# Kernel tuning notes

Measured on AMD Instinct MI355X. Metric: run time of the kernel, lower is better.

Reference implementation:

```python
import jax, jax.numpy as jnp
import numpy as np

N_NODES = 20000
N_EDGES = 320000
D = 512
CENTERS = 8
N_CLASSES = 128


def setup_inputs() -> dict:
    key = jax.random.key(0)
    k1, k2, k3, k4 = jax.random.split(key, 4)
    h = jax.random.normal(k1, (N_NODES, D), dtype=jnp.float32)
    edge_index = jax.random.randint(k2, (2, N_EDGES), 0, N_NODES, dtype=jnp.int32)
    Ws = jax.random.normal(k3, (CENTERS, D), dtype=jnp.float32) * 0.05
    Wt = jax.random.normal(k4, (CENTERS, N_CLASSES, D), dtype=jnp.float32) * 0.05
    return {"h": h, "edge_index": edge_index, "Ws": Ws, "Wt": Wt}


def reference(h, edge_index, Ws, Wt):
    N = h.shape[0]
    # add self loops (add_self_loops)
    loops = jnp.arange(N, dtype=edge_index.dtype)
    src = jnp.concatenate([edge_index[0], loops])
    dst = jnp.concatenate([edge_index[1], loops])
    # scatter-mean aggregation: agg[i] = mean_{(j->i)} h[j]
    summed = jax.ops.segment_sum(h[src], dst, num_segments=N)  # [N, D]
    cnt = jax.ops.segment_sum(jnp.ones_like(dst, dtype=h.dtype), dst, num_segments=N)
    hm = summed / cnt[:, None]  # cnt >= 1 due to self loops
    # router: argmax over structure-token scores
    scores = hm @ Ws.T                         # [N, CENTERS]
    route = jnp.argmax(scores, axis=1)         # [N]
    # hard-routed per-expert linear (compute all experts, select routed one)
    all_out = jnp.einsum('nd,cod->nco', hm, Wt)  # [N, CENTERS, N_CLASSES]
    out = jnp.take_along_axis(all_out, route[:, None, None], axis=1)[:, 0, :]
    return out
```

## Files before the change

kernel.cpp:

```cpp
#include <hip/hip_runtime.h>

#define DIM    512
#define NCLS   128
#define NCENT  8
#define TM     64
#define WSLOT  64
#define NB     64
#define KC2    64
#define KP2    72

typedef unsigned short ushort_t;
typedef unsigned int   uint_t;
typedef __attribute__((ext_vector_type(8))) short bf16x8;
typedef __attribute__((ext_vector_type(4))) float f32x4;

static __device__ __forceinline__ ushort_t f2bf(float f) {
    uint_t x = __float_as_uint(f);
    uint_t r = (x + 0x7fffu + ((x >> 16) & 1u)) >> 16;
    return (ushort_t)r;
}
static __device__ __forceinline__ float bf_lo(uint_t w) {
    return __uint_as_float(w << 16);
}
static __device__ __forceinline__ float bf_hi(uint_t w) {
    return __uint_as_float(w & 0xffff0000u);
}


__global__ __launch_bounds__(256) void prep_kernel(const float* __restrict__ h,
                                                   const float* __restrict__ Ws,
                                                   const float* __restrict__ Wt,
                                                   ushort_t* __restrict__ hb,
                                                   float* __restrict__ q,
                                                   ushort_t* __restrict__ wtb,
                                                   int N, int nprep, int total8) {
    if ((int)blockIdx.x >= nprep) {
        int i = (blockIdx.x - nprep) * 256 + threadIdx.x;
        if (i < total8) {
            const float* src = Wt + (size_t)i * 8;
            float4 a = *(const float4*)src;
            float4 b = *(const float4*)(src + 4);
            union { ushort_t us[8]; uint4 v; } pk;
            pk.us[0] = f2bf(a.x); pk.us[1] = f2bf(a.y);
            pk.us[2] = f2bf(a.z); pk.us[3] = f2bf(a.w);
            pk.us[4] = f2bf(b.x); pk.us[5] = f2bf(b.y);
            pk.us[6] = f2bf(b.z); pk.us[7] = f2bf(b.w);
            *(uint4*)(wtb + (size_t)i * 8) = pk.v;
        }
        return;
    }
    int wid = (blockIdx.x * 256 + threadIdx.x) >> 6;
    int lane = threadIdx.x & 63;
    if (wid >= N) return;

    const float* row = h + (size_t)wid * DIM + lane * 8;
    float4 a = *(const float4*)row;
    float4 b = *(const float4*)(row + 4);
    float fa[8] = {a.x, a.y, a.z, a.w, b.x, b.y, b.z, b.w};

    union { ushort_t us[8]; uint4 v; } pk;
    #pragma unroll
    for (int i = 0; i < 8; ++i) pk.us[i] = f2bf(fa[i]);
    *(uint4*)(hb + (size_t)wid * DIM + lane * 8) = pk.v;

    float qv = 0.f;
    #pragma unroll
    for (int c = 0; c < NCENT; ++c) {
        const float* w = Ws + c * DIM + lane * 8;
        float4 w0 = *(const float4*)w;
        float4 w1 = *(const float4*)(w + 4);
        float p = fa[0]*w0.x + fa[1]*w0.y + fa[2]*w0.z + fa[3]*w0.w
                + fa[4]*w1.x + fa[5]*w1.y + fa[6]*w1.z + fa[7]*w1.w;
        #pragma unroll
        for (int s = 32; s > 0; s >>= 1) p += __shfl_xor(p, s, 64);
        if (lane == c) qv = p;
    }
    if (lane < NCENT) q[(size_t)wid * NCENT + lane] = qv;
}


__global__ __launch_bounds__(256) void scatter_pad_kernel(const int* __restrict__ src,
                                                          const int* __restrict__ dst,
                                                          int* __restrict__ cnt,
                                                          int* __restrict__ slots, int E) {
    int i = blockIdx.x * 256 + threadIdx.x;
    if (i < E) {
        int d = dst[i];
        int k = atomicAdd(&cnt[d], 1);
        if (k < WSLOT) slots[(size_t)d * WSLOT + k] = src[i];
    }
}


__global__ __launch_bounds__(256) void gather_route_kernel(
        const ushort_t* __restrict__ hb, const int* __restrict__ cnt,
        const int* __restrict__ slots, const float* __restrict__ q,
        ushort_t* __restrict__ hmb, int* __restrict__ route, int N) {
    int wid = (blockIdx.x * 256 + threadIdx.x) >> 6;
    int lane = threadIdx.x & 63;
    if (wid >= N) return;

    int cn = cnt[wid]; if (cn > WSLOT) cn = WSLOT;
    int myslot = (lane < cn) ? slots[(size_t)wid * WSLOT + lane] : 0;

    float qs[NCENT];
    if (lane < cn) {
        const float* qr = q + (size_t)myslot * NCENT;
        float4 q0 = *(const float4*)qr;
        float4 q1 = *(const float4*)(qr + 4);
        qs[0]=q0.x; qs[1]=q0.y; qs[2]=q0.z; qs[3]=q0.w;
        qs[4]=q1.x; qs[5]=q1.y; qs[6]=q1.z; qs[7]=q1.w;
    } else {
        #pragma unroll
        for (int c = 0; c < NCENT; ++c) qs[c] = 0.f;
    }

    float acc[8];
    {
        uint4 u = *(const uint4*)(hb + (size_t)wid * DIM + lane * 8);
        acc[0] = bf_lo(u.x); acc[1] = bf_hi(u.x);
        acc[2] = bf_lo(u.y); acc[3] = bf_hi(u.y);
        acc[4] = bf_lo(u.z); acc[5] = bf_hi(u.z);
        acc[6] = bf_lo(u.w); acc[7] = bf_hi(u.w);
    }
    int j = 0;
    for (; j + 8 <= cn; j += 8) {
        uint4 u[8];
        #pragma unroll
        for (int k = 0; k < 8; ++k) {
            int s = __shfl(myslot, j + k, 64);
            u[k] = *(const uint4*)(hb + (size_t)s * DIM + lane * 8);
        }
        #pragma unroll
        for (int k = 0; k < 8; ++k) {
            acc[0] += bf_lo(u[k].x); acc[1] += bf_hi(u[k].x);
            acc[2] += bf_lo(u[k].y); acc[3] += bf_hi(u[k].y);
            acc[4] += bf_lo(u[k].z); acc[5] += bf_hi(u[k].z);
            acc[6] += bf_lo(u[k].w); acc[7] += bf_hi(u[k].w);
        }
    }
    for (; j < cn; ++j) {
        int s = __shfl(myslot, j, 64);
        uint4 u = *(const uint4*)(hb + (size_t)s * DIM + lane * 8);
        acc[0] += bf_lo(u.x); acc[1] += bf_hi(u.x);
        acc[2] += bf_lo(u.y); acc[3] += bf_hi(u.y);
        acc[4] += bf_lo(u.z); acc[5] += bf_hi(u.z);
        acc[6] += bf_lo(u.w); acc[7] += bf_hi(u.w);
    }
    float inv = 1.0f / (float)(cn + 1);
    union { ushort_t us[8]; uint4 v; } pk;
    #pragma unroll
    for (int k = 0; k < 8; ++k) pk.us[k] = f2bf(acc[k] * inv);
    *(uint4*)(hmb + (size_t)wid * DIM + lane * 8) = pk.v;

    #pragma unroll
    for (int c = 0; c < NCENT; ++c) {
        float v = qs[c];
        #pragma unroll
        for (int s = 32; s > 0; s >>= 1) v += __shfl_xor(v, s, 64);
        qs[c] = v;
    }
    if (lane == 0) {
        const float* qn = q + (size_t)wid * NCENT;
        int best = 0; float bv = qs[0] + qn[0];
        #pragma unroll
        for (int c = 1; c < NCENT; ++c) {
            float v = qs[c] + qn[c];
            if (v > bv) { bv = v; best = c; }
        }
        route[wid] = best;
    }
}


__global__ __launch_bounds__(256) void route_hist_kernel(const int* __restrict__ route,
                                                         int* __restrict__ bhist, int N) {
    __shared__ int lh[NCENT];
    int t = threadIdx.x;
    if (t < NCENT) lh[t] = 0;
    __syncthreads();
    for (int i = blockIdx.x * 256 + t; i < N; i += NB * 256)
        atomicAdd(&lh[route[i]], 1);
    __syncthreads();
    if (t < NCENT) bhist[blockIdx.x * NCENT + t] = lh[t];
}


__global__ __launch_bounds__(512) void scan_bins_kernel(const int* __restrict__ bhist,
                                                        int* __restrict__ bbase,
                                                        int* __restrict__ goff,
                                                        int* __restrict__ tloff) {
    __shared__ int s[NCENT][NB];
    __shared__ int go[NCENT + 1], tl[NCENT + 1];
    int t = threadIdx.x;
    int b = t >> 3, c = t & 7;
    int v = bhist[b * NCENT + c];
    s[c][b] = v;
    __syncthreads();
    for (int st = 1; st < NB; st <<= 1) {
        int a = (b >= st) ? s[c][b - st] : 0;
        __syncthreads();
        s[c][b] += a;
        __syncthreads();
    }
    if (t == 0) {
        int g = 0, tt = 0;
        for (int cc = 0; cc < NCENT; ++cc) {
            go[cc] = g; tl[cc] = tt;
            int gc = s[cc][NB - 1];
            g += gc; tt += (gc + TM - 1) / TM;
        }
        go[NCENT] = g; tl[NCENT] = tt;
    }
    __syncthreads();
    bbase[b * NCENT + c] = go[c] + s[c][b] - v;
    if (t < NCENT + 1) { goff[t] = go[t]; tloff[t] = tl[t]; }
}


__global__ __launch_bounds__(256) void group_scatter2_kernel(
        const int* __restrict__ route, const int* __restrict__ bbase,
        int* __restrict__ nlist, int N) {
    __shared__ int lcur[NCENT];
    int t = threadIdx.x;
    if (t < NCENT) lcur[t] = bbase[blockIdx.x * NCENT + t];
    __syncthreads();
    for (int i = blockIdx.x * 256 + t; i < N; i += NB * 256) {
        int p = atomicAdd(&lcur[route[i]], 1);
        nlist[p] = i;
    }
}


__global__ __launch_bounds__(256) void gemm_mfma_kernel(
        const ushort_t* __restrict__ hmb, const int* __restrict__ nlist,
        const int* __restrict__ goff, const int* __restrict__ tloff,
        const ushort_t* __restrict__ wtb, float* __restrict__ out) {
    __shared__ ushort_t a_s[TM * KP2];
    __shared__ ushort_t b_s[NCLS * KP2];
    __shared__ int nl_s[TM];

    int b = blockIdx.x;
    if (b >= tloff[NCENT]) return;
    int c = 0;
    while (b >= tloff[c + 1]) ++c;
    int row0 = goff[c] + (b - tloff[c]) * TM;
    int mrows = goff[c + 1] - row0; if (mrows > TM) mrows = TM;

    int tid = threadIdx.x;
    int wv = tid >> 6;
    int lane = tid & 63;

    if (tid < TM) nl_s[tid] = nlist[row0 + (tid < mrows ? tid : mrows - 1)];
    __syncthreads();

    f32x4 acc[8];
    #pragma unroll
    for (int t = 0; t < 8; ++t) acc[t] = (f32x4){0.f, 0.f, 0.f, 0.f};

    const ushort_t* wt_c = wtb + (size_t)c * NCLS * DIM;

    for (int k0 = 0; k0 < DIM; k0 += KC2) {
        #pragma unroll
        for (int r = 0; r < 2; ++r) {
            int idx = tid + 256 * r;
            int row = idx >> 3;
            int kq = (idx & 7) * 8;
            int nd = nl_s[row];
            uint4 v = *(const uint4*)(hmb + (size_t)nd * DIM + k0 + kq);
            *(uint4*)&a_s[row * KP2 + kq] = v;
        }
        #pragma unroll
        for (int r = 0; r < 4; ++r) {
            int idx = tid + 256 * r;
            int row = idx >> 3;
            int kq = (idx & 7) * 8;
            uint4 v = *(const uint4*)(wt_c + (size_t)row * DIM + k0 + kq);
            *(uint4*)&b_s[row * KP2 + kq] = v;
        }
        __syncthreads();
        #pragma unroll
        for (int s = 0; s < 2; ++s) {
            int kof = s * 32 + (lane >> 4) * 8;
            bf16x8 af = *(const bf16x8*)&a_s[(wv * 16 + (lane & 15)) * KP2 + kof];
            #pragma unroll
            for (int t = 0; t < 8; ++t) {
                bf16x8 bf = *(const bf16x8*)&b_s[(t * 16 + (lane & 15)) * KP2 + kof];
                acc[t] = __builtin_amdgcn_mfma_f32_16x16x32_bf16(af, bf, acc[t], 0, 0, 0);
            }
        }
        __syncthreads();
    }

    #pragma unroll
    for (int r4 = 0; r4 < 4; ++r4) {
        int row = wv * 16 + (lane >> 4) * 4 + r4;
        if (row < mrows) {
            int nd = nl_s[row];
            float* orow = out + (size_t)nd * NCLS + (lane & 15);
            #pragma unroll
            for (int t = 0; t < 8; ++t)
                orow[t * 16] = acc[t][r4];
        }
    }
}


__global__ __launch_bounds__(256) void node_kernel(const float* __restrict__ h,
                                                   const int* __restrict__ cnt,
                                                   const int* __restrict__ slots,
                                                   const float* __restrict__ Ws,
                                                   const float* __restrict__ Wt,
                                                   float* __restrict__ out) {
    int node = blockIdx.x;
    int t = threadIdx.x;
    __shared__ float hm[DIM];
    __shared__ float sc[NCENT];
    __shared__ int route_s;

    int d0 = t * 2;
    float2 acc = *(const float2*)(h + (size_t)node * DIM + d0);
    int cn = cnt[node]; if (cn > WSLOT) cn = WSLOT;
    const int* sl = slots + (size_t)node * WSLOT;
    for (int j = 0; j < cn; ++j) {
        float2 v = *(const float2*)(h + (size_t)sl[j] * DIM + d0);
        acc.x += v.x; acc.y += v.y;
    }
    float inv = 1.0f / (float)(cn + 1);
    hm[d0] = acc.x * inv; hm[d0 + 1] = acc.y * inv;
    __syncthreads();
    if (t < NCENT) {
        const float* w = Ws + t * DIM;
        float s = 0.f;
        for (int d = 0; d < DIM; d += 4) {
            float4 a = *(const float4*)(&hm[d]);
            float4 b = *(const float4*)(w + d);
            s += a.x * b.x + a.y * b.y + a.z * b.z + a.w * b.w;
        }
        sc[t] = s;
    }
    __syncthreads();
    if (t == 0) {
        int best = 0; float bv = sc[0];
        #pragma unroll
        for (int c = 1; c < NCENT; ++c)
            if (sc[c] > bv) { bv = sc[c]; best = c; }
        route_s = best;
    }
    __syncthreads();
    int route = route_s;
    if (t < NCLS) {
        const float* w = Wt + ((size_t)route * NCLS + t) * DIM;
        float s = 0.f;
        for (int d = 0; d < DIM; d += 4) {
            float4 a = *(const float4*)(&hm[d]);
            float4 b = *(const float4*)(w + d);
            s += a.x * b.x + a.y * b.y + a.z * b.z + a.w * b.w;
        }
        out[(size_t)node * NCLS + t] = s;
    }
}


extern "C" void kernel_launch(void* const* d_in, const int* in_sizes, int n_in,
                              void* d_out, int out_size, void* d_ws, size_t ws_size,
                              hipStream_t stream) {
    const float* h   = (const float*)d_in[0];
    const int*   ei  = (const int*)d_in[1];
    const float* Ws  = (const float*)d_in[2];
    const float* Wt  = (const float*)d_in[3];
    float*       out = (float*)d_out;

    int N = in_sizes[0] / DIM;
    int E = in_sizes[1] / 2;
    int wt_elems = in_sizes[3];
    const int* esrc = ei;
    const int* edst = ei + E;

    int* wsp    = (int*)d_ws;
    int* cnt    = wsp;
    int* route  = cnt + N;
    int* goff   = route + N;
    int* tloff  = goff + NCENT + 1;
    int* bhist  = tloff + NCENT + 1;
    int* bbase  = bhist + NB * NCENT;
    int* nlist  = bbase + NB * NCENT;
    int* slots  = nlist + N;
    size_t iw   = (size_t)(3 * N) + 2 * (NCENT + 1) + 2 * NB * NCENT
                + (size_t)N * WSLOT;
    size_t q_off  = ((iw * 4 + 255) & ~(size_t)255);
    float* q    = (float*)((char*)d_ws + q_off);
    size_t hb_off = ((q_off + (size_t)N * NCENT * 4 + 255) & ~(size_t)255);
    ushort_t* hb = (ushort_t*)((char*)d_ws + hb_off);
    size_t hmb_off = ((hb_off + (size_t)N * DIM * 2 + 255) & ~(size_t)255);
    ushort_t* hmb = (ushort_t*)((char*)d_ws + hmb_off);
    size_t wtb_off = ((hmb_off + (size_t)N * DIM * 2 + 255) & ~(size_t)255);
    ushort_t* wtb = (ushort_t*)((char*)d_ws + wtb_off);
    size_t need = wtb_off + (size_t)wt_elems * 2;

    hipMemsetAsync(cnt, 0, (size_t)N * sizeof(int), stream);

    if (ws_size >= need) {
        int nprep = (N + 3) / 4;
        int total8 = wt_elems / 8;
        int nwt = (total8 + 255) / 256;
        prep_kernel<<<nprep + nwt, 256, 0, stream>>>(h, Ws, Wt, hb, q, wtb,
                                                     N, nprep, total8);
        scatter_pad_kernel<<<(E + 255) / 256, 256, 0, stream>>>(esrc, edst, cnt, slots, E);
        gather_route_kernel<<<(N + 3) / 4, 256, 0, stream>>>(hb, cnt, slots, q,
                                                             hmb, route, N);
        route_hist_kernel<<<NB, 256, 0, stream>>>(route, bhist, N);
        scan_bins_kernel<<<1, 512, 0, stream>>>(bhist, bbase, goff, tloff);
        group_scatter2_kernel<<<NB, 256, 0, stream>>>(route, bbase, nlist, N);
        int maxtiles = N / TM + NCENT + 1;
        gemm_mfma_kernel<<<maxtiles, 256, 0, stream>>>(hmb, nlist, goff, tloff, wtb, out);
    } else {
        scatter_pad_kernel<<<(E + 255) / 256, 256, 0, stream>>>(esrc, edst, cnt, slots, E);
        node_kernel<<<N, 256, 0, stream>>>(h, cnt, slots, Ws, Wt, out);
    }
}
```

Baseline: 114.3 us.

## Fuse edge scatter into prep and scan into group scatter; deepen gather prefetch

Merges the edge-slot scatter into the prep kernel as extra blocks, and folds the single-block bin scan into the per-block group-scatter kernel, where each block redundantly recomputes the prefix. Together these remove two kernel launches and their serialization gaps. The gather kernel also issues up to 16 neighbor row loads up front before accumulating, to raise memory-level parallelism for typical degrees (~17). The costs are more registers in the gather kernel and redundant scan work in each of the 64 blocks.

```diff
diff --git a/kernel.cpp b/kernel.cpp
--- a/kernel.cpp
+++ b/kernel.cpp
@@ -27,36 +27,46 @@
 }
 
 
-__global__ __launch_bounds__(256) void prep_kernel(const float* __restrict__ h,
-                                                   const float* __restrict__ Ws,
-                                                   const float* __restrict__ Wt,
-                                                   ushort_t* __restrict__ hb,
-                                                   float* __restrict__ q,
-                                                   ushort_t* __restrict__ wtb,
-                                                   int N, int nprep, int total8) {
-    if ((int)blockIdx.x >= nprep) {
-        int i = (blockIdx.x - nprep) * 256 + threadIdx.x;
+__global__ __launch_bounds__(256) void fused_prep_kernel(
+        const float* __restrict__ h, const float* __restrict__ Ws,
+        const float* __restrict__ Wt, const int* __restrict__ esrc,
+        const int* __restrict__ edst, ushort_t* __restrict__ hb,
+        float* __restrict__ q, ushort_t* __restrict__ wtb,
+        int* __restrict__ cnt, int* __restrict__ slots,
+        int N, int E, int nprep, int nwt, int total8) {
+    int b = blockIdx.x;
+    if (b >= nprep + nwt) {
+        int i = (b - nprep - nwt) * 256 + threadIdx.x;
+        if (i < E) {
+            int d = edst[i];
+            int k = atomicAdd(&cnt[d], 1);
+            if (k < WSLOT) slots[(size_t)d * WSLOT + k] = esrc[i];
+        }
+        return;
+    }
+    if (b >= nprep) {
+        int i = (b - nprep) * 256 + threadIdx.x;
         if (i < total8) {
             const float* src = Wt + (size_t)i * 8;
             float4 a = *(const float4*)src;
-            float4 b = *(const float4*)(src + 4);
+            float4 bb = *(const float4*)(src + 4);
             union { ushort_t us[8]; uint4 v; } pk;
-            pk.us[0] = f2bf(a.x); pk.us[1] = f2bf(a.y);
-            pk.us[2] = f2bf(a.z); pk.us[3] = f2bf(a.w);
-            pk.us[4] = f2bf(b.x); pk.us[5] = f2bf(b.y);
-            pk.us[6] = f2bf(b.z); pk.us[7] = f2bf(b.w);
+            pk.us[0] = f2bf(a.x);  pk.us[1] = f2bf(a.y);
+            pk.us[2] = f2bf(a.z);  pk.us[3] = f2bf(a.w);
+            pk.us[4] = f2bf(bb.x); pk.us[5] = f2bf(bb.y);
+            pk.us[6] = f2bf(bb.z); pk.us[7] = f2bf(bb.w);
             *(uint4*)(wtb + (size_t)i * 8) = pk.v;
         }
         return;
     }
-    int wid = (blockIdx.x * 256 + threadIdx.x) >> 6;
+    int wid = (b * 256 + threadIdx.x) >> 6;
     int lane = threadIdx.x & 63;
     if (wid >= N) return;
 
     const float* row = h + (size_t)wid * DIM + lane * 8;
     float4 a = *(const float4*)row;
-    float4 b = *(const float4*)(row + 4);
-    float fa[8] = {a.x, a.y, a.z, a.w, b.x, b.y, b.z, b.w};
+    float4 bb = *(const float4*)(row + 4);
+    float fa[8] = {a.x, a.y, a.z, a.w, bb.x, bb.y, bb.z, bb.w};
 
     union { ushort_t us[8]; uint4 v; } pk;
     #pragma unroll
@@ -76,19 +86,6 @@
         if (lane == c) qv = p;
     }
     if (lane < NCENT) q[(size_t)wid * NCENT + lane] = qv;
-}
-
-
-__global__ __launch_bounds__(256) void scatter_pad_kernel(const int* __restrict__ src,
-                                                          const int* __restrict__ dst,
-                                                          int* __restrict__ cnt,
-                                                          int* __restrict__ slots, int E) {
-    int i = blockIdx.x * 256 + threadIdx.x;
-    if (i < E) {
-        int d = dst[i];
-        int k = atomicAdd(&cnt[d], 1);
-        if (k < WSLOT) slots[(size_t)d * WSLOT + k] = src[i];
-    }
 }
 
 
@@ -115,37 +112,52 @@
         for (int c = 0; c < NCENT; ++c) qs[c] = 0.f;
     }
 
+    uint4 su = *(const uint4*)(hb + (size_t)wid * DIM + lane * 8);
+    uint4 u[16];
+    int m = cn < 16 ? cn : 16;
+    #pragma unroll
+    for (int k = 0; k < 16; ++k) {
+        int s = __shfl(myslot, k, 64);
+        if (k < m) u[k] = *(const uint4*)(hb + (size_t)s * DIM + lane * 8);
+    }
+
     float acc[8];
-    {
-        uint4 u = *(const uint4*)(hb + (size_t)wid * DIM + lane * 8);
-        acc[0] = bf_lo(u.x); acc[1] = bf_hi(u.x);
-        acc[2] = bf_lo(u.y); acc[3] = bf_hi(u.y);
-        acc[4] = bf_lo(u.z); acc[5] = bf_hi(u.z);
-        acc[6] = bf_lo(u.w); acc[7] = bf_hi(u.w);
-    }
-    int j = 0;
-    for (; j + 8 <= cn; j += 8) {
-        uint4 u[8];
-        #pragma unroll
-        for (int k = 0; k < 8; ++k) {
-            int s = __shfl(myslot, j + k, 64);
-            u[k] = *(const uint4*)(hb + (size_t)s * DIM + lane * 8);
-        }
-        #pragma unroll
-        for (int k = 0; k < 8; ++k) {
+    acc[0] = bf_lo(su.x); acc[1] = bf_hi(su.x);
+    acc[2] = bf_lo(su.y); acc[3] = bf_hi(su.y);
+    acc[4] = bf_lo(su.z); acc[5] = bf_hi(su.z);
+    acc[6] = bf_lo(su.w); acc[7] = bf_hi(su.w);
+    #pragma unroll
+    for (int k = 0; k < 16; ++k) {
+        if (k < m) {
             acc[0] += bf_lo(u[k].x); acc[1] += bf_hi(u[k].x);
             acc[2] += bf_lo(u[k].y); acc[3] += bf_hi(u[k].y);
             acc[4] += bf_lo(u[k].z); acc[5] += bf_hi(u[k].z);
             acc[6] += bf_lo(u[k].w); acc[7] += bf_hi(u[k].w);
         }
     }
+    int j = 16;
+    for (; j + 8 <= cn; j += 8) {
+        uint4 v[8];
+        #pragma unroll
+        for (int k = 0; k < 8; ++k) {
+            int s = __shfl(myslot, j + k, 64);
+            v[k] = *(const uint4*)(hb + (size_t)s * DIM + lane * 8);
+        }
+        #pragma unroll
+        for (int k = 0; k < 8; ++k) {
+            acc[0] += bf_lo(v[k].x); acc[1] += bf_hi(v[k].x);
+            acc[2] += bf_lo(v[k].y); acc[3] += bf_hi(v[k].y);
+            acc[4] += bf_lo(v[k].z); acc[5] += bf_hi(v[k].z);
+            acc[6] += bf_lo(v[k].w); acc[7] += bf_hi(v[k].w);
+        }
+    }
     for (; j < cn; ++j) {
         int s = __shfl(myslot, j, 64);
-        uint4 u = *(const uint4*)(hb + (size_t)s * DIM + lane * 8);
-        acc[0] += bf_lo(u.x); acc[1] += bf_hi(u.x);
-        acc[2] += bf_lo(u.y); acc[3] += bf_hi(u.y);
-        acc[4] += bf_lo(u.z); acc[5] += bf_hi(u.z);
-        acc[6] += bf_lo(u.w); acc[7] += bf_hi(u.w);
+        uint4 v = *(const uint4*)(hb + (size_t)s * DIM + lane * 8);
+        acc[0] += bf_lo(v.x); acc[1] += bf_hi(v.x);
+        acc[2] += bf_lo(v.y); acc[3] += bf_hi(v.y);
+        acc[4] += bf_lo(v.z); acc[5] += bf_hi(v.z);
+        acc[6] += bf_lo(v.w); acc[7] += bf_hi(v.w);
     }
     float inv = 1.0f / (float)(cn + 1);
     union { ushort_t us[8]; uint4 v; } pk;
@@ -186,49 +198,44 @@
 }
 
 
-__global__ __launch_bounds__(512) void scan_bins_kernel(const int* __restrict__ bhist,
-                                                        int* __restrict__ bbase,
-                                                        int* __restrict__ goff,
-                                                        int* __restrict__ tloff) {
-    __shared__ int s[NCENT][NB];
+__global__ __launch_bounds__(256) void scan_scatter_kernel(
+        const int* __restrict__ bhist, const int* __restrict__ route,
+        int* __restrict__ nlist, int* __restrict__ goff,
+        int* __restrict__ tloff, int N) {
+    __shared__ int bh[NB * NCENT];
+    __shared__ int pre[NB][NCENT];
     __shared__ int go[NCENT + 1], tl[NCENT + 1];
+    __shared__ int lcur[NCENT];
     int t = threadIdx.x;
-    int b = t >> 3, c = t & 7;
-    int v = bhist[b * NCENT + c];
-    s[c][b] = v;
-    __syncthreads();
-    for (int st = 1; st < NB; st <<= 1) {
-        int a = (b >= st) ? s[c][b - st] : 0;
-        __syncthreads();
-        s[c][b] += a;
-        __syncthreads();
-    }
+
+    for (int i = t; i < NB * NCENT; i += 256) bh[i] = bhist[i];
+    __syncthreads();
+    if (t < NCENT) {
+        int run = 0;
+        for (int b = 0; b < NB; ++b) {
+            pre[b][t] = run;
+            run += bh[b * NCENT + t];
+        }
+        go[t] = run;
+    }
+    __syncthreads();
     if (t == 0) {
         int g = 0, tt = 0;
-        for (int cc = 0; cc < NCENT; ++cc) {
-            go[cc] = g; tl[cc] = tt;
-            int gc = s[cc][NB - 1];
+        for (int c = 0; c < NCENT; ++c) {
+            int gc = go[c];
+            go[c] = g; tl[c] = tt;
             g += gc; tt += (gc + TM - 1) / TM;
         }
         go[NCENT] = g; tl[NCENT] = tt;
     }
     __syncthreads();
-    bbase[b * NCENT + c] = go[c] + s[c][b] - v;
-    if (t < NCENT + 1) { goff[t] = go[t]; tloff[t] = tl[t]; }
-}
-
-
-__global__ __launch_bounds__(256) void group_scatter2_kernel(
-        const int* __restrict__ route, const int* __restrict__ bbase,
-        int* __restrict__ nlist, int N) {
-    __shared__ int lcur[NCENT];
-    int t = threadIdx.x;
-    if (t < NCENT) lcur[t] = bbase[blockIdx.x * NCENT + t];
+    if (t < NCENT) lcur[t] = go[t] + pre[blockIdx.x][t];
     __syncthreads();
     for (int i = blockIdx.x * 256 + t; i < N; i += NB * 256) {
         int p = atomicAdd(&lcur[route[i]], 1);
         nlist[p] = i;
     }
+    if (blockIdx.x == 0 && t < NCENT + 1) { goff[t] = go[t]; tloff[t] = tl[t]; }
 }
 
 
@@ -383,10 +390,9 @@
     int* goff   = route + N;
     int* tloff  = goff + NCENT + 1;
     int* bhist  = tloff + NCENT + 1;
-    int* bbase  = bhist + NB * NCENT;
-    int* nlist  = bbase + NB * NCENT;
+    int* nlist  = bhist + NB * NCENT;
     int* slots  = nlist + N;
-    size_t iw   = (size_t)(3 * N) + 2 * (NCENT + 1) + 2 * NB * NCENT
+    size_t iw   = (size_t)(3 * N) + 2 * (NCENT + 1) + NB * NCENT
                 + (size_t)N * WSLOT;
     size_t q_off  = ((iw * 4 + 255) & ~(size_t)255);
     float* q    = (float*)((char*)d_ws + q_off);
@@ -404,18 +410,21 @@
         int nprep = (N + 3) / 4;
         int total8 = wt_elems / 8;
         int nwt = (total8 + 255) / 256;
-        prep_kernel<<<nprep + nwt, 256, 0, stream>>>(h, Ws, Wt, hb, q, wtb,
-                                                     N, nprep, total8);
-        scatter_pad_kernel<<<(E + 255) / 256, 256, 0, stream>>>(esrc, edst, cnt, slots, E);
+        int nsc = (E + 255) / 256;
+        fused_prep_kernel<<<nprep + nwt + nsc, 256, 0, stream>>>(
+            h, Ws, Wt, esrc, edst, hb, q, wtb, cnt, slots,
+            N, E, nprep, nwt, total8);
         gather_route_kernel<<<(N + 3) / 4, 256, 0, stream>>>(hb, cnt, slots, q,
                                                              hmb, route, N);
         route_hist_kernel<<<NB, 256, 0, stream>>>(route, bhist, N);
-        scan_bins_kernel<<<1, 512, 0, stream>>>(bhist, bbase, goff, tloff);
-        group_scatter2_kernel<<<NB, 256, 0, stream>>>(route, bbase, nlist, N);
+        scan_scatter_kernel<<<NB, 256, 0, stream>>>(bhist, route, nlist,
+                                                    goff, tloff, N);
         int maxtiles = N / TM + NCENT + 1;
         gemm_mfma_kernel<<<maxtiles, 256, 0, stream>>>(hmb, nlist, goff, tloff, wtb, out);
     } else {
-        scatter_pad_kernel<<<(E + 255) / 256, 256, 0, stream>>>(esrc, edst, cnt, slots, E);
+        fused_prep_kernel<<<0 + 0 + (E + 255) / 256, 256, 0, stream>>>(
+            h, Ws, Wt, esrc, edst, (ushort_t*)nullptr, (float*)nullptr,
+            (ushort_t*)nullptr, cnt, slots, N, E, 0, 0, 0);
         node_kernel<<<N, 256, 0, stream>>>(h, cnt, slots, Ws, Wt, out);
     }
 }
```

New measurement: 117.8 us. 3.1% more time.
